# Performance work log

Hardware: AMD Instinct MI355X
Metric: run time of the kernel (lower is better)

## Reference

```python
import jax, jax.numpy as jnp
import numpy as np

N_NODES = 50000
N_EDGES = 800000
N_FEAT, N_HID, N_LATENT = 512, 256, 128


def spmm(rows, cols, vals, dense):
    # out[r] += vals[e] * dense[cols[e]]  -- COO SpMM via segment_sum
    gathered = dense[cols] * vals[:, None]          # [E, d]
    return jax.ops.segment_sum(gathered, rows, num_segments=N_NODES)


def setup_inputs() -> dict:
    key = jax.random.key(0)
    ks = jax.random.split(key, 8)
    x = jax.random.normal(ks[0], (N_NODES, N_FEAT), dtype=jnp.float32)
    edge_rows = jax.random.randint(ks[1], (N_EDGES,), 0, N_NODES, dtype=jnp.int32)
    edge_cols = jax.random.randint(ks[2], (N_EDGES,), 0, N_NODES, dtype=jnp.int32)
    edge_vals = jax.random.uniform(ks[3], (N_EDGES,), dtype=jnp.float32)
    # Glorot-style init like the torch GraphConvolution
    W1 = jax.random.normal(ks[4], (N_FEAT, N_HID), dtype=jnp.float32) / np.sqrt(N_FEAT)
    b1 = jnp.zeros((N_HID,), dtype=jnp.float32)
    W2 = jax.random.normal(ks[5], (N_HID, N_LATENT), dtype=jnp.float32) / np.sqrt(N_HID)
    b2 = jnp.zeros((N_LATENT,), dtype=jnp.float32)
    return {"x": x, "edge_rows": edge_rows, "edge_cols": edge_cols,
            "edge_vals": edge_vals, "W1": W1, "b1": b1, "W2": W2, "b2": b2}


def reference(x, edge_rows, edge_cols, edge_vals, W1, b1, W2, b2):
    # layer 1: relu(adj @ (x @ W1) + b1)
    h = spmm(edge_rows, edge_cols, edge_vals, x @ W1) + b1
    h = jax.nn.relu(h)
    # layer 2: relu(adj @ (h @ W2) + b2)
    z = spmm(edge_rows, edge_cols, edge_vals, h @ W2) + b2
    return jax.nn.relu(z)
```

## Files before the change

kernel.cpp:

```cpp
#include <hip/hip_runtime.h>
#include <hip/hip_bf16.h>


typedef __attribute__((ext_vector_type(8))) short bf16x8;
typedef __attribute__((ext_vector_type(8))) unsigned short ushort8;
typedef __attribute__((ext_vector_type(4))) float f32x4;

#define NN 50000
#define NE 800000
#define NF 512
#define NH 256
#define NL 128
#define NB ((NN + 255) / 256)

static __device__ __forceinline__ unsigned short f2bf(float f) {
  union { float f; unsigned int u; } v; v.f = f;
  unsigned int r = v.u + 0x7fffu + ((v.u >> 16) & 1u);
  return (unsigned short)(r >> 16);
}
static __device__ __forceinline__ float bf2f(unsigned short u) {
  union { unsigned int u; float f; } v; v.u = (unsigned int)u << 16;
  return v.f;
}

static __device__ __forceinline__ void gll16(const void* g, void* l) {
  __builtin_amdgcn_global_load_lds(
      (const __attribute__((address_space(1))) void*)g,
      (__attribute__((address_space(3))) void*)l, 16, 0, 0);
}

extern "C" __global__ void k_hist(const int* __restrict__ rows, int* __restrict__ counts, int n) {
  int i = blockIdx.x * 256 + threadIdx.x;
  if (i < n) atomicAdd(&counts[rows[i]], 1);
}

extern "C" __global__ __launch_bounds__(256) void k_blocksum(
    const int* __restrict__ counts, int* __restrict__ bsum, int n) {
  __shared__ int s[256];
  int t = threadIdx.x;
  int i = blockIdx.x * 256 + t;
  s[t] = (i < n) ? counts[i] : 0;
  __syncthreads();
  for (int off = 128; off > 0; off >>= 1) {
    if (t < off) s[t] += s[t + off];
    __syncthreads();
  }
  if (t == 0) bsum[blockIdx.x] = s[0];
}

extern "C" __global__ __launch_bounds__(256) void k_scansums(
    const int* __restrict__ bsum, int* __restrict__ bpre, int* __restrict__ rp, int nb, int n) {
  __shared__ int s[256];
  int t = threadIdx.x;
  int v = (t < nb) ? bsum[t] : 0;
  s[t] = v;
  __syncthreads();
  for (int off = 1; off < 256; off <<= 1) {
    int u = (t >= off) ? s[t - off] : 0;
    __syncthreads();
    s[t] += u;
    __syncthreads();
  }
  if (t < nb) bpre[t] = s[t] - v;
  if (t == 255) rp[n] = s[255];
}

extern "C" __global__ __launch_bounds__(256) void k_scanfin(
    const int* __restrict__ counts, const int* __restrict__ bpre,
    int* __restrict__ rp, int* __restrict__ cur, int n) {
  __shared__ int s[256];
  int t = threadIdx.x;
  int i = blockIdx.x * 256 + t;
  int c = (i < n) ? counts[i] : 0;
  s[t] = c;
  __syncthreads();
  for (int off = 1; off < 256; off <<= 1) {
    int u = (t >= off) ? s[t - off] : 0;
    __syncthreads();
    s[t] += u;
    __syncthreads();
  }
  if (i < n) {
    int e = bpre[blockIdx.x] + s[t] - c;
    rp[i] = e;
    cur[i] = e;
  }
}

extern "C" __global__ void k_scatter(const int* __restrict__ rows, const int* __restrict__ cols,
    const float* __restrict__ vals, int* __restrict__ cur, int2* __restrict__ ep, int n) {
  int i = blockIdx.x * 256 + threadIdx.x;
  if (i < n) {
    int p = atomicAdd(&cur[rows[i]], 1);
    int2 e; e.x = cols[i]; e.y = __float_as_int(vals[i]);
    ep[p] = e;
  }
}

extern "C" __global__ void k_transcast(const float* __restrict__ w, unsigned short* __restrict__ wt,
                                       int K, int N) {
  int k = blockIdx.x; int n = threadIdx.x;
  wt[(size_t)n * K + k] = f2bf(w[(size_t)k * N + n]);
}

extern "C" __global__ __launch_bounds__(256) void k_gemm1(
    const float* __restrict__ A, const unsigned short* __restrict__ BT,
    unsigned short* __restrict__ C) {
  __shared__ __align__(16) unsigned short sA[128 * 64];
  __shared__ __align__(16) unsigned short sB[128 * 64];
  int tid = threadIdx.x;
  int lane = tid & 63, wid = tid >> 6;
  int wm = (wid >> 1) * 64, wn = (wid & 1) * 64;
  int bm = blockIdx.x * 128, bn = blockIdx.y * 128;
  int l15 = lane & 15, lq = lane >> 4;
  int swzbase = l15 & 7;
  f32x4 acc[4][4];
#pragma unroll
  for (int i = 0; i < 4; ++i)
#pragma unroll
    for (int j = 0; j < 4; ++j) acc[i][j] = (f32x4){0.f, 0.f, 0.f, 0.f};

  for (int k0 = 0; k0 < NF; k0 += 64) {
#pragma unroll
    for (int j = 0; j < 4; ++j) {
      int u = tid + 256 * j;
      int row = u >> 3, cu = u & 7;
      int ga = bm + row; if (ga >= NN) ga = NN - 1;
      const float* src = A + (size_t)ga * NF + k0 + cu * 8;
      float4 f0 = *(const float4*)src;
      float4 f1 = *(const float4*)(src + 4);
      ushort8 o;
      o[0] = f2bf(f0.x); o[1] = f2bf(f0.y); o[2] = f2bf(f0.z); o[3] = f2bf(f0.w);
      o[4] = f2bf(f1.x); o[5] = f2bf(f1.y); o[6] = f2bf(f1.z); o[7] = f2bf(f1.w);
      *(ushort8*)(&sA[row * 64 + (cu ^ (row & 7)) * 8]) = o;
    }
#pragma unroll
    for (int j = 0; j < 4; ++j) {
      int u = tid + 256 * j;
      int row = u >> 3, cu = u & 7;
      int g = cu ^ (row & 7);
      gll16(BT + (size_t)(bn + row) * NF + k0 + g * 8, &sB[u * 8]);
    }
    __syncthreads();
#pragma unroll
    for (int ks = 0; ks < 64; ks += 32) {
      bf16x8 af[4], bfr[4];
#pragma unroll
      for (int t = 0; t < 4; ++t) {
        int sz = (((ks >> 3) + lq) ^ swzbase) * 8;
        af[t]  = *(const bf16x8*)(&sA[(wm + t * 16 + l15) * 64 + sz]);
        bfr[t] = *(const bf16x8*)(&sB[(wn + t * 16 + l15) * 64 + sz]);
      }
#pragma unroll
      for (int mt = 0; mt < 4; ++mt)
#pragma unroll
        for (int nt = 0; nt < 4; ++nt)
          acc[mt][nt] = __builtin_amdgcn_mfma_f32_16x16x32_bf16(af[mt], bfr[nt], acc[mt][nt], 0, 0, 0);
    }
    __syncthreads();
  }
#pragma unroll
  for (int mt = 0; mt < 4; ++mt) {
#pragma unroll
    for (int r = 0; r < 4; ++r) {
      int gr = bm + wm + mt * 16 + lq * 4 + r;
      if (gr < NN) {
#pragma unroll
        for (int nt = 0; nt < 4; ++nt) {
          int gc = bn + wn + nt * 16 + l15;
          C[(size_t)gr * NH + gc] = f2bf(acc[mt][nt][r]);
        }
      }
    }
  }
}

extern "C" __global__ __launch_bounds__(256) void k_gemm2(
    const unsigned short* __restrict__ A, const unsigned short* __restrict__ BT,
    unsigned short* __restrict__ C) {
  __shared__ __align__(16) unsigned short sA[64 * 64];
  __shared__ __align__(16) unsigned short sB[128 * 64];
  int tid = threadIdx.x;
  int lane = tid & 63, wid = tid >> 6;
  int wm = (wid >> 1) * 32, wn = (wid & 1) * 64;
  int bm = blockIdx.x * 64;
  int l15 = lane & 15, lq = lane >> 4;
  int swzbase = l15 & 7;
  f32x4 acc[2][4];
#pragma unroll
  for (int i = 0; i < 2; ++i)
#pragma unroll
    for (int j = 0; j < 4; ++j) acc[i][j] = (f32x4){0.f, 0.f, 0.f, 0.f};

  for (int k0 = 0; k0 < NH; k0 += 64) {
#pragma unroll
    for (int j = 0; j < 2; ++j) {
      int u = tid + 256 * j;
      int row = u >> 3, cu = u & 7;
      int ga = bm + row; if (ga >= NN) ga = NN - 1;
      int g = cu ^ (row & 7);
      gll16(A + (size_t)ga * NH + k0 + g * 8, &sA[u * 8]);
    }
#pragma unroll
    for (int j = 0; j < 4; ++j) {
      int u = tid + 256 * j;
      int row = u >> 3, cu = u & 7;
      int g = cu ^ (row & 7);
      gll16(BT + (size_t)row * NH + k0 + g * 8, &sB[u * 8]);
    }
    __syncthreads();
#pragma unroll
    for (int ks = 0; ks < 64; ks += 32) {
      bf16x8 af[2], bfr[4];
#pragma unroll
      for (int t = 0; t < 2; ++t)
        af[t] = *(const bf16x8*)(&sA[(wm + t * 16 + l15) * 64 + (((ks >> 3) + lq) ^ swzbase) * 8]);
#pragma unroll
      for (int t = 0; t < 4; ++t)
        bfr[t] = *(const bf16x8*)(&sB[(wn + t * 16 + l15) * 64 + (((ks >> 3) + lq) ^ swzbase) * 8]);
#pragma unroll
      for (int mt = 0; mt < 2; ++mt)
#pragma unroll
        for (int nt = 0; nt < 4; ++nt)
          acc[mt][nt] = __builtin_amdgcn_mfma_f32_16x16x32_bf16(af[mt], bfr[nt], acc[mt][nt], 0, 0, 0);
    }
    __syncthreads();
  }
#pragma unroll
  for (int mt = 0; mt < 2; ++mt) {
#pragma unroll
    for (int r = 0; r < 4; ++r) {
      int gr = bm + wm + mt * 16 + lq * 4 + r;
      if (gr < NN) {
#pragma unroll
        for (int nt = 0; nt < 4; ++nt) {
          int gc = wn + nt * 16 + l15;
          C[(size_t)gr * NL + gc] = f2bf(acc[mt][nt][r]);
        }
      }
    }
  }
}

extern "C" __global__ __launch_bounds__(256) void k_spmm256(
    const int* __restrict__ rp, const int2* __restrict__ ep,
    const unsigned short* __restrict__ src, const float* __restrict__ bias,
    ushort4* __restrict__ out) {
  int row = blockIdx.x * 4 + (threadIdx.x >> 6);
  int lane = threadIdx.x & 63;
  if (row >= NN) return;
  int e0 = __builtin_amdgcn_readfirstlane(rp[row]);
  int e1 = __builtin_amdgcn_readfirstlane(rp[row + 1]);
  const ushort4* srcv = (const ushort4*)src;
  float4 acc = {0.f, 0.f, 0.f, 0.f};
  int e = e0;
  for (; e + 8 <= e1; e += 8) {
    int2 p[8]; ushort4 g[8];
#pragma unroll
    for (int j = 0; j < 8; ++j) p[j] = ep[e + j];
#pragma unroll
    for (int j = 0; j < 8; ++j) g[j] = srcv[(size_t)p[j].x * (NH / 4) + lane];
#pragma unroll
    for (int j = 0; j < 8; ++j) {
      float v = __int_as_float(p[j].y);
      acc.x = fmaf(v, bf2f(g[j].x), acc.x); acc.y = fmaf(v, bf2f(g[j].y), acc.y);
      acc.z = fmaf(v, bf2f(g[j].z), acc.z); acc.w = fmaf(v, bf2f(g[j].w), acc.w);
    }
  }
  for (; e + 4 <= e1; e += 4) {
    int2 p[4]; ushort4 g[4];
#pragma unroll
    for (int j = 0; j < 4; ++j) p[j] = ep[e + j];
#pragma unroll
    for (int j = 0; j < 4; ++j) g[j] = srcv[(size_t)p[j].x * (NH / 4) + lane];
#pragma unroll
    for (int j = 0; j < 4; ++j) {
      float v = __int_as_float(p[j].y);
      acc.x = fmaf(v, bf2f(g[j].x), acc.x); acc.y = fmaf(v, bf2f(g[j].y), acc.y);
      acc.z = fmaf(v, bf2f(g[j].z), acc.z); acc.w = fmaf(v, bf2f(g[j].w), acc.w);
    }
  }
  for (; e < e1; ++e) {
    int2 p = ep[e];
    float v = __int_as_float(p.y);
    ushort4 g = srcv[(size_t)p.x * (NH / 4) + lane];
    acc.x = fmaf(v, bf2f(g.x), acc.x); acc.y = fmaf(v, bf2f(g.y), acc.y);
    acc.z = fmaf(v, bf2f(g.z), acc.z); acc.w = fmaf(v, bf2f(g.w), acc.w);
  }
  float4 b = ((const float4*)bias)[lane];
  ushort4 o;
  o.x = f2bf(fmaxf(acc.x + b.x, 0.f));
  o.y = f2bf(fmaxf(acc.y + b.y, 0.f));
  o.z = f2bf(fmaxf(acc.z + b.z, 0.f));
  o.w = f2bf(fmaxf(acc.w + b.w, 0.f));
  out[(size_t)row * (NH / 4) + lane] = o;
}

extern "C" __global__ __launch_bounds__(256) void k_spmm128(
    const int* __restrict__ rp, const int2* __restrict__ ep,
    const unsigned short* __restrict__ src, const float* __restrict__ bias,
    float2* __restrict__ out) {
  int row = blockIdx.x * 4 + (threadIdx.x >> 6);
  int lane = threadIdx.x & 63;
  if (row >= NN) return;
  int e0 = __builtin_amdgcn_readfirstlane(rp[row]);
  int e1 = __builtin_amdgcn_readfirstlane(rp[row + 1]);
  const ushort2* srcv = (const ushort2*)src;
  float2 acc = {0.f, 0.f};
  int e = e0;
  for (; e + 8 <= e1; e += 8) {
    int2 p[8]; ushort2 g[8];
#pragma unroll
    for (int j = 0; j < 8; ++j) p[j] = ep[e + j];
#pragma unroll
    for (int j = 0; j < 8; ++j) g[j] = srcv[(size_t)p[j].x * (NL / 2) + lane];
#pragma unroll
    for (int j = 0; j < 8; ++j) {
      float v = __int_as_float(p[j].y);
      acc.x = fmaf(v, bf2f(g[j].x), acc.x); acc.y = fmaf(v, bf2f(g[j].y), acc.y);
    }
  }
  for (; e + 4 <= e1; e += 4) {
    int2 p[4]; ushort2 g[4];
#pragma unroll
    for (int j = 0; j < 4; ++j) p[j] = ep[e + j];
#pragma unroll
    for (int j = 0; j < 4; ++j) g[j] = srcv[(size_t)p[j].x * (NL / 2) + lane];
#pragma unroll
    for (int j = 0; j < 4; ++j) {
      float v = __int_as_float(p[j].y);
      acc.x = fmaf(v, bf2f(g[j].x), acc.x); acc.y = fmaf(v, bf2f(g[j].y), acc.y);
    }
  }
  for (; e < e1; ++e) {
    int2 p = ep[e];
    float v = __int_as_float(p.y);
    ushort2 g = srcv[(size_t)p.x * (NL / 2) + lane];
    acc.x = fmaf(v, bf2f(g.x), acc.x); acc.y = fmaf(v, bf2f(g.y), acc.y);
  }
  float2 b = ((const float2*)bias)[lane];
  float2 o;
  o.x = fmaxf(acc.x + b.x, 0.f);
  o.y = fmaxf(acc.y + b.y, 0.f);
  out[(size_t)row * (NL / 2) + lane] = o;
}

extern "C" void kernel_launch(void* const* d_in, const int* in_sizes, int n_in,
                              void* d_out, int out_size, void* d_ws, size_t ws_size,
                              hipStream_t stream) {
  const float* x   = (const float*)d_in[0];
  const int* erow  = (const int*)d_in[1];
  const int* ecol  = (const int*)d_in[2];
  const float* ev  = (const float*)d_in[3];
  const float* W1  = (const float*)d_in[4];
  const float* b1  = (const float*)d_in[5];
  const float* W2  = (const float*)d_in[6];
  const float* b2  = (const float*)d_in[7];

  char* ws = (char*)d_ws;
  unsigned short* xwb = (unsigned short*)(ws + 0);
  unsigned short* hbf = (unsigned short*)(ws + 25600000);
  unsigned short* hwb = (unsigned short*)(ws + 51200000);
  unsigned short* w1t = (unsigned short*)(ws + 64000000);
  unsigned short* w2t = (unsigned short*)(ws + 64262144);
  int* rp    = (int*)(ws + 64327680);
  int* cur   = (int*)(ws + 64528384);
  int* cnt   = (int*)(ws + 64729088);
  int* bsum  = (int*)(ws + 64929792);
  int* bpre  = (int*)(ws + 64930816);
  int2* ep   = (int2*)(ws + 64931840);

  hipMemsetAsync(cnt, 0, NN * sizeof(int), stream);
  k_hist<<<NE / 256, 256, 0, stream>>>(erow, cnt, NE);
  k_blocksum<<<NB, 256, 0, stream>>>(cnt, bsum, NN);
  k_scansums<<<1, 256, 0, stream>>>(bsum, bpre, rp, NB, NN);
  k_scanfin<<<NB, 256, 0, stream>>>(cnt, bpre, rp, cur, NN);
  k_scatter<<<NE / 256, 256, 0, stream>>>(erow, ecol, ev, cur, ep, NE);

  k_transcast<<<NF, NH, 0, stream>>>(W1, w1t, NF, NH);
  k_gemm1<<<dim3((NN + 127) / 128, NH / 128), 256, 0, stream>>>(x, w1t, xwb);
  k_spmm256<<<NN / 4, 256, 0, stream>>>(rp, ep, xwb, b1, (ushort4*)hbf);

  k_transcast<<<NH, NL, 0, stream>>>(W2, w2t, NH, NL);
  k_gemm2<<<(NN + 63) / 64, 256, 0, stream>>>(hbf, w2t, hwb);
  k_spmm128<<<NN / 4, 256, 0, stream>>>(rp, ep, hwb, b2, (float2*)d_out);
}
```

Baseline: 376.7 us.

## Double-buffer shared memory in both GEMM kernels to overlap loads with MFMA

Both dense GEMM kernels now use two LDS buffers. Each kernel prefetches the next K-tile (register loads of fp32 A plus async global_load_lds for B) while the MFMAs run on the current tile, and drops one barrier per iteration. The aim is to hide global memory latency behind compute. In exchange, LDS use doubles and gemm1 needs extra registers for the prefetched fp32 values, which may lower occupancy. The GEMMs are only part of the total time, next to the SpMM stages.

```diff
diff --git a/kernel.cpp b/kernel.cpp
--- a/kernel.cpp
+++ b/kernel.cpp
@@ -21,6 +21,13 @@
 static __device__ __forceinline__ float bf2f(unsigned short u) {
   union { unsigned int u; float f; } v; v.u = (unsigned int)u << 16;
   return v.f;
+}
+
+static __device__ __forceinline__ ushort8 cvt8(float4 a, float4 b) {
+  ushort8 o;
+  o[0] = f2bf(a.x); o[1] = f2bf(a.y); o[2] = f2bf(a.z); o[3] = f2bf(a.w);
+  o[4] = f2bf(b.x); o[5] = f2bf(b.y); o[6] = f2bf(b.z); o[7] = f2bf(b.w);
+  return o;
 }
 
 static __device__ __forceinline__ void gll16(const void* g, void* l) {
@@ -106,8 +113,8 @@
 extern "C" __global__ __launch_bounds__(256) void k_gemm1(
     const float* __restrict__ A, const unsigned short* __restrict__ BT,
     unsigned short* __restrict__ C) {
-  __shared__ __align__(16) unsigned short sA[128 * 64];
-  __shared__ __align__(16) unsigned short sB[128 * 64];
+  __shared__ __align__(16) unsigned short sA[2][128 * 64];
+  __shared__ __align__(16) unsigned short sB[2][128 * 64];
   int tid = threadIdx.x;
   int lane = tid & 63, wid = tid >> 6;
   int wm = (wid >> 1) * 64, wn = (wid & 1) * 64;
@@ -120,36 +127,61 @@
 #pragma unroll
     for (int j = 0; j < 4; ++j) acc[i][j] = (f32x4){0.f, 0.f, 0.f, 0.f};
 
-  for (int k0 = 0; k0 < NF; k0 += 64) {
-#pragma unroll
-    for (int j = 0; j < 4; ++j) {
-      int u = tid + 256 * j;
-      int row = u >> 3, cu = u & 7;
-      int ga = bm + row; if (ga >= NN) ga = NN - 1;
-      const float* src = A + (size_t)ga * NF + k0 + cu * 8;
-      float4 f0 = *(const float4*)src;
-      float4 f1 = *(const float4*)(src + 4);
-      ushort8 o;
-      o[0] = f2bf(f0.x); o[1] = f2bf(f0.y); o[2] = f2bf(f0.z); o[3] = f2bf(f0.w);
-      o[4] = f2bf(f1.x); o[5] = f2bf(f1.y); o[6] = f2bf(f1.z); o[7] = f2bf(f1.w);
-      *(ushort8*)(&sA[row * 64 + (cu ^ (row & 7)) * 8]) = o;
-    }
-#pragma unroll
-    for (int j = 0; j < 4; ++j) {
-      int u = tid + 256 * j;
-      int row = u >> 3, cu = u & 7;
-      int g = cu ^ (row & 7);
-      gll16(BT + (size_t)(bn + row) * NF + k0 + g * 8, &sB[u * 8]);
-    }
-    __syncthreads();
+  float4 ra[4][2];
+
+#pragma unroll
+  for (int j = 0; j < 4; ++j) {
+    int u = tid + 256 * j;
+    int row = u >> 3, cu = u & 7;
+    int ga = bm + row; if (ga >= NN) ga = NN - 1;
+    const float* src = A + (size_t)ga * NF + cu * 8;
+    ra[j][0] = ((const float4*)src)[0];
+    ra[j][1] = ((const float4*)src)[1];
+  }
+#pragma unroll
+  for (int j = 0; j < 4; ++j) {
+    int u = tid + 256 * j;
+    int row = u >> 3, cu = u & 7;
+    int g = cu ^ (row & 7);
+    gll16(BT + (size_t)(bn + row) * NF + g * 8, &sB[0][u * 8]);
+  }
+#pragma unroll
+  for (int j = 0; j < 4; ++j) {
+    int u = tid + 256 * j;
+    int row = u >> 3, cu = u & 7;
+    *(ushort8*)(&sA[0][row * 64 + (cu ^ (row & 7)) * 8]) = cvt8(ra[j][0], ra[j][1]);
+  }
+  __syncthreads();
+
+  int cur = 0;
+  for (int t = 0; t < NF / 64; ++t) {
+    int k1 = (t + 1) * 64;
+    if (t < NF / 64 - 1) {
+#pragma unroll
+      for (int j = 0; j < 4; ++j) {
+        int u = tid + 256 * j;
+        int row = u >> 3, cu = u & 7;
+        int ga = bm + row; if (ga >= NN) ga = NN - 1;
+        const float* src = A + (size_t)ga * NF + k1 + cu * 8;
+        ra[j][0] = ((const float4*)src)[0];
+        ra[j][1] = ((const float4*)src)[1];
+      }
+#pragma unroll
+      for (int j = 0; j < 4; ++j) {
+        int u = tid + 256 * j;
+        int row = u >> 3, cu = u & 7;
+        int g = cu ^ (row & 7);
+        gll16(BT + (size_t)(bn + row) * NF + k1 + g * 8, &sB[cur ^ 1][u * 8]);
+      }
+    }
 #pragma unroll
     for (int ks = 0; ks < 64; ks += 32) {
       bf16x8 af[4], bfr[4];
 #pragma unroll
-      for (int t = 0; t < 4; ++t) {
+      for (int tt = 0; tt < 4; ++tt) {
         int sz = (((ks >> 3) + lq) ^ swzbase) * 8;
-        af[t]  = *(const bf16x8*)(&sA[(wm + t * 16 + l15) * 64 + sz]);
-        bfr[t] = *(const bf16x8*)(&sB[(wn + t * 16 + l15) * 64 + sz]);
+        af[tt]  = *(const bf16x8*)(&sA[cur][(wm + tt * 16 + l15) * 64 + sz]);
+        bfr[tt] = *(const bf16x8*)(&sB[cur][(wn + tt * 16 + l15) * 64 + sz]);
       }
 #pragma unroll
       for (int mt = 0; mt < 4; ++mt)
@@ -157,7 +189,16 @@
         for (int nt = 0; nt < 4; ++nt)
           acc[mt][nt] = __builtin_amdgcn_mfma_f32_16x16x32_bf16(af[mt], bfr[nt], acc[mt][nt], 0, 0, 0);
     }
-    __syncthreads();
+    if (t < NF / 64 - 1) {
+#pragma unroll
+      for (int j = 0; j < 4; ++j) {
+        int u = tid + 256 * j;
+        int row = u >> 3, cu = u & 7;
+        *(ushort8*)(&sA[cur ^ 1][row * 64 + (cu ^ (row & 7)) * 8]) = cvt8(ra[j][0], ra[j][1]);
+      }
+    }
+    __syncthreads();
+    cur ^= 1;
   }
 #pragma unroll
   for (int mt = 0; mt < 4; ++mt) {
@@ -178,8 +219,8 @@
 extern "C" __global__ __launch_bounds__(256) void k_gemm2(
     const unsigned short* __restrict__ A, const unsigned short* __restrict__ BT,
     unsigned short* __restrict__ C) {
-  __shared__ __align__(16) unsigned short sA[64 * 64];
-  __shared__ __align__(16) unsigned short sB[128 * 64];
+  __shared__ __align__(16) unsigned short sA[2][64 * 64];
+  __shared__ __align__(16) unsigned short sB[2][128 * 64];
   int tid = threadIdx.x;
   int lane = tid & 63, wid = tid >> 6;
   int wm = (wid >> 1) * 32, wn = (wid & 1) * 64;
@@ -192,32 +233,52 @@
 #pragma unroll
     for (int j = 0; j < 4; ++j) acc[i][j] = (f32x4){0.f, 0.f, 0.f, 0.f};
 
-  for (int k0 = 0; k0 < NH; k0 += 64) {
-#pragma unroll
-    for (int j = 0; j < 2; ++j) {
-      int u = tid + 256 * j;
-      int row = u >> 3, cu = u & 7;
-      int ga = bm + row; if (ga >= NN) ga = NN - 1;
-      int g = cu ^ (row & 7);
-      gll16(A + (size_t)ga * NH + k0 + g * 8, &sA[u * 8]);
-    }
-#pragma unroll
-    for (int j = 0; j < 4; ++j) {
-      int u = tid + 256 * j;
-      int row = u >> 3, cu = u & 7;
-      int g = cu ^ (row & 7);
-      gll16(BT + (size_t)row * NH + k0 + g * 8, &sB[u * 8]);
-    }
-    __syncthreads();
+#pragma unroll
+  for (int j = 0; j < 2; ++j) {
+    int u = tid + 256 * j;
+    int row = u >> 3, cu = u & 7;
+    int ga = bm + row; if (ga >= NN) ga = NN - 1;
+    int g = cu ^ (row & 7);
+    gll16(A + (size_t)ga * NH + g * 8, &sA[0][u * 8]);
+  }
+#pragma unroll
+  for (int j = 0; j < 4; ++j) {
+    int u = tid + 256 * j;
+    int row = u >> 3, cu = u & 7;
+    int g = cu ^ (row & 7);
+    gll16(BT + (size_t)row * NH + g * 8, &sB[0][u * 8]);
+  }
+  __syncthreads();
+
+  int cur = 0;
+  for (int t = 0; t < NH / 64; ++t) {
+    int k1 = (t + 1) * 64;
+    if (t < NH / 64 - 1) {
+#pragma unroll
+      for (int j = 0; j < 2; ++j) {
+        int u = tid + 256 * j;
+        int row = u >> 3, cu = u & 7;
+        int ga = bm + row; if (ga >= NN) ga = NN - 1;
+        int g = cu ^ (row & 7);
+        gll16(A + (size_t)ga * NH + k1 + g * 8, &sA[cur ^ 1][u * 8]);
+      }
+#pragma unroll
+      for (int j = 0; j < 4; ++j) {
+        int u = tid + 256 * j;
+        int row = u >> 3, cu = u & 7;
+        int g = cu ^ (row & 7);
+        gll16(BT + (size_t)row * NH + k1 + g * 8, &sB[cur ^ 1][u * 8]);
+      }
+    }
 #pragma unroll
     for (int ks = 0; ks < 64; ks += 32) {
       bf16x8 af[2], bfr[4];
 #pragma unroll
-      for (int t = 0; t < 2; ++t)
-        af[t] = *(const bf16x8*)(&sA[(wm + t * 16 + l15) * 64 + (((ks >> 3) + lq) ^ swzbase) * 8]);
-#pragma unroll
-      for (int t = 0; t < 4; ++t)
-        bfr[t] = *(const bf16x8*)(&sB[(wn + t * 16 + l15) * 64 + (((ks >> 3) + lq) ^ swzbase) * 8]);
+      for (int tt = 0; tt < 2; ++tt)
+        af[tt] = *(const bf16x8*)(&sA[cur][(wm + tt * 16 + l15) * 64 + (((ks >> 3) + lq) ^ swzbase) * 8]);
+#pragma unroll
+      for (int tt = 0; tt < 4; ++tt)
+        bfr[tt] = *(const bf16x8*)(&sB[cur][(wn + tt * 16 + l15) * 64 + (((ks >> 3) + lq) ^ swzbase) * 8]);
 #pragma unroll
       for (int mt = 0; mt < 2; ++mt)
 #pragma unroll
@@ -225,6 +286,7 @@
           acc[mt][nt] = __builtin_amdgcn_mfma_f32_16x16x32_bf16(af[mt], bfr[nt], acc[mt][nt], 0, 0, 0);
     }
     __syncthreads();
+    cur ^= 1;
   }
 #pragma unroll
   for (int mt = 0; mt < 2; ++mt) {
```

Result: no change. 382.3 us (+1.5%).

## Replace LDS-tiled GEMMs with register-direct MFMA loads and packed bf16 convert

Applied to the files above, without the earlier changes.

Both dense GEMMs drop shared-memory staging and barriers. Each wave now loads its A fragment straight from global memory with a double-buffered register prefetch, and reads B (the small transposed weights) directly from global memory, where it is expected to stay cached. The fp32-to-bf16 conversion of x uses the packed v_cvt_pk_bf16_f32 instruction instead of software rounding, and the gemm1 grid is reordered so the two column blocks of the same rows run next to each other. This is meant to remove LDS traffic and sync overhead, at the cost of more global or L2 loads for B and no sharing of data across waves.

```diff
diff --git a/kernel.cpp b/kernel.cpp
--- a/kernel.cpp
+++ b/kernel.cpp
@@ -3,7 +3,6 @@
 
 
 typedef __attribute__((ext_vector_type(8))) short bf16x8;
-typedef __attribute__((ext_vector_type(8))) unsigned short ushort8;
 typedef __attribute__((ext_vector_type(4))) float f32x4;
 
 #define NN 50000
@@ -23,10 +22,16 @@
   return v.f;
 }
 
-static __device__ __forceinline__ void gll16(const void* g, void* l) {
-  __builtin_amdgcn_global_load_lds(
-      (const __attribute__((address_space(1))) void*)g,
-      (__attribute__((address_space(3))) void*)l, 16, 0, 0);
+static __device__ __forceinline__ unsigned int pkbf(float lo, float hi) {
+  unsigned int r;
+  asm("v_cvt_pk_bf16_f32 %0, %1, %2" : "=v"(r) : "v"(lo), "v"(hi));
+  return r;
+}
+static __device__ __forceinline__ uint4 pk8(float4 a, float4 b) {
+  uint4 o;
+  o.x = pkbf(a.x, a.y); o.y = pkbf(a.z, a.w);
+  o.z = pkbf(b.x, b.y); o.w = pkbf(b.z, b.w);
+  return o;
 }
 
 extern "C" __global__ void k_hist(const int* __restrict__ rows, int* __restrict__ counts, int n) {
@@ -106,137 +111,120 @@
 extern "C" __global__ __launch_bounds__(256) void k_gemm1(
     const float* __restrict__ A, const unsigned short* __restrict__ BT,
     unsigned short* __restrict__ C) {
-  __shared__ __align__(16) unsigned short sA[128 * 64];
-  __shared__ __align__(16) unsigned short sB[128 * 64];
   int tid = threadIdx.x;
   int lane = tid & 63, wid = tid >> 6;
-  int wm = (wid >> 1) * 64, wn = (wid & 1) * 64;
-  int bm = blockIdx.x * 128, bn = blockIdx.y * 128;
   int l15 = lane & 15, lq = lane >> 4;
-  int swzbase = l15 & 7;
-  f32x4 acc[4][4];
-#pragma unroll
-  for (int i = 0; i < 4; ++i)
-#pragma unroll
-    for (int j = 0; j < 4; ++j) acc[i][j] = (f32x4){0.f, 0.f, 0.f, 0.f};
-
-  for (int k0 = 0; k0 < NF; k0 += 64) {
-#pragma unroll
-    for (int j = 0; j < 4; ++j) {
-      int u = tid + 256 * j;
-      int row = u >> 3, cu = u & 7;
-      int ga = bm + row; if (ga >= NN) ga = NN - 1;
-      const float* src = A + (size_t)ga * NF + k0 + cu * 8;
-      float4 f0 = *(const float4*)src;
-      float4 f1 = *(const float4*)(src + 4);
-      ushort8 o;
-      o[0] = f2bf(f0.x); o[1] = f2bf(f0.y); o[2] = f2bf(f0.z); o[3] = f2bf(f0.w);
-      o[4] = f2bf(f1.x); o[5] = f2bf(f1.y); o[6] = f2bf(f1.z); o[7] = f2bf(f1.w);
-      *(ushort8*)(&sA[row * 64 + (cu ^ (row & 7)) * 8]) = o;
-    }
-#pragma unroll
-    for (int j = 0; j < 4; ++j) {
-      int u = tid + 256 * j;
-      int row = u >> 3, cu = u & 7;
-      int g = cu ^ (row & 7);
-      gll16(BT + (size_t)(bn + row) * NF + k0 + g * 8, &sB[u * 8]);
-    }
-    __syncthreads();
-#pragma unroll
-    for (int ks = 0; ks < 64; ks += 32) {
-      bf16x8 af[4], bfr[4];
-#pragma unroll
-      for (int t = 0; t < 4; ++t) {
-        int sz = (((ks >> 3) + lq) ^ swzbase) * 8;
-        af[t]  = *(const bf16x8*)(&sA[(wm + t * 16 + l15) * 64 + sz]);
-        bfr[t] = *(const bf16x8*)(&sB[(wn + t * 16 + l15) * 64 + sz]);
+  int bn = blockIdx.x * 128, bm = blockIdx.y * 64;
+
+  int arow = bm + wid * 16 + l15; if (arow >= NN) arow = NN - 1;
+  const float* ap = A + (size_t)arow * NF + lq * 8;
+  const unsigned short* bp[8];
+#pragma unroll
+  for (int nt = 0; nt < 8; ++nt)
+    bp[nt] = BT + (size_t)(bn + nt * 16 + l15) * NF + lq * 8;
+
+  f32x4 acc[8];
+#pragma unroll
+  for (int i = 0; i < 8; ++i) acc[i] = (f32x4){0.f, 0.f, 0.f, 0.f};
+
+  float4 apf[2][4];
+#pragma unroll
+  for (int ks = 0; ks < 2; ++ks) {
+    apf[0][ks * 2 + 0] = *(const float4*)(ap + ks * 32);
+    apf[0][ks * 2 + 1] = *(const float4*)(ap + ks * 32 + 4);
+  }
+
+#pragma unroll
+  for (int t = 0; t < 8; ++t) {
+    int k0 = t * 64;
+    if (t < 7) {
+#pragma unroll
+      for (int ks = 0; ks < 2; ++ks) {
+        apf[(t + 1) & 1][ks * 2 + 0] = *(const float4*)(ap + k0 + 64 + ks * 32);
+        apf[(t + 1) & 1][ks * 2 + 1] = *(const float4*)(ap + k0 + 64 + ks * 32 + 4);
       }
-#pragma unroll
-      for (int mt = 0; mt < 4; ++mt)
-#pragma unroll
-        for (int nt = 0; nt < 4; ++nt)
-          acc[mt][nt] = __builtin_amdgcn_mfma_f32_16x16x32_bf16(af[mt], bfr[nt], acc[mt][nt], 0, 0, 0);
-    }
-    __syncthreads();
-  }
-#pragma unroll
-  for (int mt = 0; mt < 4; ++mt) {
+    }
+#pragma unroll
+    for (int ks = 0; ks < 2; ++ks) {
+      bf16x8 bfr[8];
+#pragma unroll
+      for (int nt = 0; nt < 8; ++nt)
+        bfr[nt] = *(const bf16x8*)(bp[nt] + k0 + ks * 32);
+      union { uint4 u; bf16x8 v; } cv;
+      cv.u = pk8(apf[t & 1][ks * 2], apf[t & 1][ks * 2 + 1]);
+      bf16x8 af = cv.v;
+#pragma unroll
+      for (int nt = 0; nt < 8; ++nt)
+        acc[nt] = __builtin_amdgcn_mfma_f32_16x16x32_bf16(af, bfr[nt], acc[nt], 0, 0, 0);
+    }
+  }
+
+#pragma unroll
+  for (int nt = 0; nt < 8; ++nt) {
 #pragma unroll
     for (int r = 0; r < 4; ++r) {
-      int gr = bm + wm + mt * 16 + lq * 4 + r;
+      int gr = bm + wid * 16 + lq * 4 + r;
       if (gr < NN) {
-#pragma unroll
-        for (int nt = 0; nt < 4; ++nt) {
-          int gc = bn + wn + nt * 16 + l15;
-          C[(size_t)gr * NH + gc] = f2bf(acc[mt][nt][r]);
-        }
+        int gc = bn + nt * 16 + l15;
+        C[(size_t)gr * NH + gc] = f2bf(acc[nt][r]);
       }
     }
   }
 }
 
 extern "C" __global__ __launch_bounds__(256) void k_gemm2(
-    const unsigned short* __restrict__ A, const unsigned short* __restrict__ BT,
+    const unsigned short* __restrict__ Ah, const unsigned short* __restrict__ BT,
     unsigned short* __restrict__ C) {
-  __shared__ __align__(16) unsigned short sA[64 * 64];
-  __shared__ __align__(16) unsigned short sB[128 * 64];
   int tid = threadIdx.x;
   int lane = tid & 63, wid = tid >> 6;
-  int wm = (wid >> 1) * 32, wn = (wid & 1) * 64;
+  int l15 = lane & 15, lq = lane >> 4;
   int bm = blockIdx.x * 64;
-  int l15 = lane & 15, lq = lane >> 4;
-  int swzbase = l15 & 7;
-  f32x4 acc[2][4];
-#pragma unroll
-  for (int i = 0; i < 2; ++i)
-#pragma unroll
-    for (int j = 0; j < 4; ++j) acc[i][j] = (f32x4){0.f, 0.f, 0.f, 0.f};
-
-  for (int k0 = 0; k0 < NH; k0 += 64) {
-#pragma unroll
-    for (int j = 0; j < 2; ++j) {
-      int u = tid + 256 * j;
-      int row = u >> 3, cu = u & 7;
-      int ga = bm + row; if (ga >= NN) ga = NN - 1;
-      int g = cu ^ (row & 7);
-      gll16(A + (size_t)ga * NH + k0 + g * 8, &sA[u * 8]);
-    }
-#pragma unroll
-    for (int j = 0; j < 4; ++j) {
-      int u = tid + 256 * j;
-      int row = u >> 3, cu = u & 7;
-      int g = cu ^ (row & 7);
-      gll16(BT + (size_t)row * NH + k0 + g * 8, &sB[u * 8]);
-    }
-    __syncthreads();
-#pragma unroll
-    for (int ks = 0; ks < 64; ks += 32) {
-      bf16x8 af[2], bfr[4];
-#pragma unroll
-      for (int t = 0; t < 2; ++t)
-        af[t] = *(const bf16x8*)(&sA[(wm + t * 16 + l15) * 64 + (((ks >> 3) + lq) ^ swzbase) * 8]);
-#pragma unroll
-      for (int t = 0; t < 4; ++t)
-        bfr[t] = *(const bf16x8*)(&sB[(wn + t * 16 + l15) * 64 + (((ks >> 3) + lq) ^ swzbase) * 8]);
-#pragma unroll
-      for (int mt = 0; mt < 2; ++mt)
-#pragma unroll
-        for (int nt = 0; nt < 4; ++nt)
-          acc[mt][nt] = __builtin_amdgcn_mfma_f32_16x16x32_bf16(af[mt], bfr[nt], acc[mt][nt], 0, 0, 0);
-    }
-    __syncthreads();
-  }
-#pragma unroll
-  for (int mt = 0; mt < 2; ++mt) {
+
+  int arow = bm + wid * 16 + l15; if (arow >= NN) arow = NN - 1;
+  const unsigned short* ap = Ah + (size_t)arow * NH + lq * 8;
+  const unsigned short* bp[8];
+#pragma unroll
+  for (int nt = 0; nt < 8; ++nt)
+    bp[nt] = BT + (size_t)(nt * 16 + l15) * NH + lq * 8;
+
+  f32x4 acc[8];
+#pragma unroll
+  for (int i = 0; i < 8; ++i) acc[i] = (f32x4){0.f, 0.f, 0.f, 0.f};
+
+  bf16x8 apf[2][2];
+#pragma unroll
+  for (int ks = 0; ks < 2; ++ks)
+    apf[0][ks] = *(const bf16x8*)(ap + ks * 32);
+
+#pragma unroll
+  for (int t = 0; t < 4; ++t) {
+    int k0 = t * 64;
+    if (t < 3) {
+#pragma unroll
+      for (int ks = 0; ks < 2; ++ks)
+        apf[(t + 1) & 1][ks] = *(const bf16x8*)(ap + k0 + 64 + ks * 32);
+    }
+#pragma unroll
+    for (int ks = 0; ks < 2; ++ks) {
+      bf16x8 bfr[8];
+#pragma unroll
+      for (int nt = 0; nt < 8; ++nt)
+        bfr[nt] = *(const bf16x8*)(bp[nt] + k0 + ks * 32);
+      bf16x8 af = apf[t & 1][ks];
+#pragma unroll
+      for (int nt = 0; nt < 8; ++nt)
+        acc[nt] = __builtin_amdgcn_mfma_f32_16x16x32_bf16(af, bfr[nt], acc[nt], 0, 0, 0);
+    }
+  }
+
+#pragma unroll
+  for (int nt = 0; nt < 8; ++nt) {
 #pragma unroll
     for (int r = 0; r < 4; ++r) {
-      int gr = bm + wm + mt * 16 + lq * 4 + r;
+      int gr = bm + wid * 16 + lq * 4 + r;
       if (gr < NN) {
-#pragma unroll
-        for (int nt = 0; nt < 4; ++nt) {
-          int gc = wn + nt * 16 + l15;
-          C[(size_t)gr * NL + gc] = f2bf(acc[mt][nt][r]);
-        }
+        int gc = nt * 16 + l15;
+        C[(size_t)gr * NL + gc] = f2bf(acc[nt][r]);
       }
     }
   }
@@ -378,7 +366,7 @@
   k_scatter<<<NE / 256, 256, 0, stream>>>(erow, ecol, ev, cur, ep, NE);
 
   k_transcast<<<NF, NH, 0, stream>>>(W1, w1t, NF, NH);
-  k_gemm1<<<dim3((NN + 127) / 128, NH / 128), 256, 0, stream>>>(x, w1t, xwb);
+  k_gemm1<<<dim3(2, (NN + 63) / 64), 256, 0, stream>>>(x, w1t, xwb);
   k_spmm256<<<NN / 4, 256, 0, stream>>>(rp, ep, xwb, b1, (ushort4*)hbf);
 
   k_transcast<<<NH, NL, 0, stream>>>(W2, w2t, NH, NL);
```

Result: slower. 481.1 us (+27.7%).
